# Optimization experiments

Measured on AMD Instinct MI355X. Metric: run time of the kernel, lower is better.

## Reference

```python
import jax, jax.numpy as jnp
import numpy as np

K = 4            # kNN neighbors (edge_conv k=4)
HEADS = 4
HID = 32
NEG_SLOPE = 0.2  # PyG GATConv leaky_relu default


def knn_idx(x, k):
    # x: [N, C]. Pairwise squared distances via gram trick, self excluded.
    N = x.shape[0]
    sq = jnp.sum(x * x, axis=1)
    d = sq[:, None] + sq[None, :] - 2.0 * (x @ x.T)          # [N, N]
    r = jnp.arange(N)
    d = d.at[r, r].set(jnp.inf)                               # no self in kNN
    _, idx = jax.lax.top_k(-d, k)                             # [N, k] nearest
    return idx


def gat_layer(x, neigh, W, a_src, a_dst, b):
    # x: [N, C]; neigh: [N, k+1] (incl. self loop). PyG GATConv, concat=True.
    N = x.shape[0]
    h = (x @ W).reshape(N, HEADS, HID)                        # [N, H, D]
    asrc = jnp.einsum('nhd,hd->nh', h, a_src)                 # [N, H]
    adst = jnp.einsum('nhd,hd->nh', h, a_dst)                 # [N, H]
    e = jax.nn.leaky_relu(adst[:, None, :] + asrc[neigh], NEG_SLOPE)  # [N, k+1, H]
    attn = jax.nn.softmax(e, axis=1)                          # segment softmax (fixed fan-in)
    out = jnp.einsum('nkh,nkhd->nhd', attn, h[neigh])         # [N, H, D]
    return out.reshape(N, HEADS * HID) + b


def setup_inputs() -> dict:
    key = jax.random.key(0)
    ks = jax.random.split(key, 12)
    B, E, C = 256, 64, 32
    s = 0.1
    return {
        'x': jax.random.normal(ks[0], (B, E, C), jnp.float32),
        # DynamicEdgeConv MLP: Linear(2C->HID), ReLU, Linear(HID->HID)
        'mlp_w1': jax.random.normal(ks[1], (2 * C, HID), jnp.float32) * s,
        'mlp_b1': jnp.zeros((HID,), jnp.float32),
        'mlp_w2': jax.random.normal(ks[2], (HID, HID), jnp.float32) * s,
        'mlp_b2': jnp.zeros((HID,), jnp.float32),
        # GATConv(HID, HID, heads=HEADS, concat=True)
        'gat_w': jax.random.normal(ks[3], (C, HEADS * HID), jnp.float32) * s,
        'gat_asrc': jax.random.normal(ks[4], (HEADS, HID), jnp.float32) * s,
        'gat_adst': jax.random.normal(ks[5], (HEADS, HID), jnp.float32) * s,
        'gat_b': jnp.zeros((HEADS * HID,), jnp.float32),
        # fc: Linear(HID*HEADS -> num_classes)
        'fc_w': jax.random.normal(ks[6], (HEADS * HID, 2), jnp.float32) * s,
        'fc_b': jnp.zeros((2,), jnp.float32),
    }


def reference(x, mlp_w1, mlp_b1, mlp_w2, mlp_b2, gat_w, gat_asrc, gat_adst, gat_b, fc_w, fc_b):
    B, E, C = x.shape
    N = B * E
    xf = x.reshape(N, C)
    idx = knn_idx(xf, K)                                      # [N, K] int32
    # EdgeConv message MLP + max pool (edge_attr is discarded by the original forward)
    xi = xf[:, None, :]                                       # [N, 1, C]
    xj = xf[idx]                                              # [N, K, C]
    ef = jnp.concatenate([jnp.broadcast_to(xi, xj.shape), xj - xi], axis=-1)
    ef = jax.nn.relu(ef @ mlp_w1 + mlp_b1) @ mlp_w2 + mlp_b2
    _edge_attr = ef.max(axis=1)                               # [N, HID], unused downstream
    # GAT with self loops (PyG add_self_loops=True)
    neigh = jnp.concatenate([idx, jnp.arange(N)[:, None]], axis=1)  # [N, K+1]
    h = gat_layer(xf, neigh, gat_w, gat_asrc, gat_adst, gat_b)
    h = jax.nn.elu(h)
    h = h.reshape(B, E, HEADS * HID).mean(axis=1)             # [B, H*D]
    return h @ fc_w + fc_b                                    # [B, num_classes]
```

## Files before the change

### kernel.cpp

```cpp
#include <hip/hip_runtime.h>
#include <math.h>

#define N_PTS   16384
#define NT      1024
#define NCHUNK  32
#define JT_CH   (NT/NCHUNK)
#define SUBT    8
#define NSUB    (JT_CH/SUBT)
#define NS      16
#define JSPLIT  4

typedef __attribute__((ext_vector_type(4))) float f32x4;
typedef __attribute__((ext_vector_type(8))) _Float16 half8;

union H8 { half8 h; float4 f; };

#define MED3(a,b,c) __builtin_amdgcn_fmed3f((a),(b),(c))

#define INS4(c, A0, A1, A2, A3) {        \
  float n0_ = fmaxf(A0, c);              \
  float n1_ = MED3(A0, A1, c);           \
  float n2_ = MED3(A1, A2, c);           \
  float n3_ = MED3(A2, A3, c);           \
  A0 = n0_; A1 = n1_; A2 = n2_; A3 = n3_; }

__device__ __forceinline__ unsigned long long pack_key(float a, int j) {
  unsigned u = __float_as_uint(a);
  unsigned ord = u ^ (unsigned)(((int)u >> 31) | 0x80000000);
  unsigned m = ~ord;
  return ((unsigned long long)m << 32) | (unsigned)j;
}

__global__ __launch_bounds__(256) void k_prep(
    const float* __restrict__ x, float4* __restrict__ fragHi,
    float4* __restrict__ fragLo, float* __restrict__ nsq,
    unsigned* __restrict__ gcnt, unsigned long long* __restrict__ gbuf,
    unsigned* __restrict__ bcnt)
{
  int p = blockIdx.x * 256 + threadIdx.x;
  const float4* xp = (const float4*)(x + (size_t)p * 32);
  int tile = p >> 4, lb = p & 15;
  float sq = 0.f;
  #pragma unroll
  for (int g = 0; g < 4; ++g) {
    float4 va = xp[g * 2], vb = xp[g * 2 + 1];
    float f[8] = {va.x, va.y, va.z, va.w, vb.x, vb.y, vb.z, vb.w};
    H8 hh, hl;
    #pragma unroll
    for (int e = 0; e < 8; ++e) {
      sq = fmaf(f[e], f[e], sq);
      _Float16 hi = (_Float16)f[e];
      _Float16 lo = (_Float16)(f[e] - (float)hi);
      hh.h[e] = hi; hl.h[e] = lo;
    }
    int a = tile * 64 + g * 16 + lb;
    fragHi[a] = hh.f; fragLo[a] = hl.f;
  }
  nsq[p] = -0.5f * sq;
  gcnt[p] = 0u;
  #pragma unroll
  for (int e = 0; e < NS; ++e) gbuf[(size_t)p * NS + e] = ~0ull;
  if (blockIdx.x == 0 && threadIdx.x < NCHUNK) bcnt[threadIdx.x] = 0u;
}

__global__ __launch_bounds__(256, 4) void k_knnA(
    const float4* __restrict__ fragHi, const float4* __restrict__ fragLo,
    const float* __restrict__ nsq, float* __restrict__ cvals)
{
  __shared__ half8 sHi[SUBT * 64];
  __shared__ half8 sLo[SUBT * 64];
  __shared__ float sNq[SUBT * 16];

  const int tid = threadIdx.x;
  const int w = tid >> 6, lane = tid & 63;
  const int grp = lane >> 4, col = lane & 15;
  const int cy = blockIdx.y;
  const int itbase = blockIdx.x * 16 + w * 4;
  const bool blkdiag = ((int)(blockIdx.x >> 1) == cy);

  const half8* fH8 = (const half8*)fragHi;
  const half8* fL8 = (const half8*)fragLo;

  half8 bh[4], bl[4];
  #pragma unroll
  for (int s = 0; s < 4; ++s) {
    bh[s] = fH8[(size_t)(itbase + s) * 64 + lane];
    bl[s] = fL8[(size_t)(itbase + s) * 64 + lane];
  }
  const bool dg0 = (col == grp * 4 + 0), dg1 = (col == grp * 4 + 1);
  const bool dg2 = (col == grp * 4 + 2), dg3 = (col == grp * 4 + 3);

  float La1[4];
  #pragma unroll
  for (int s = 0; s < 4; ++s) La1[s] = -3.4e38f;

  for (int sc = 0; sc < NSUB; ++sc) {
    int jt0 = cy * JT_CH + sc * SUBT;
    __syncthreads();
    const float4* gH = fragHi + (size_t)jt0 * 64;
    const float4* gL = fragLo + (size_t)jt0 * 64;
    float4* dH = (float4*)sHi;
    float4* dL = (float4*)sLo;
    #pragma unroll
    for (int r = 0; r < 2; ++r) {
      dH[tid + r * 256] = gH[tid + r * 256];
      dL[tid + r * 256] = gL[tid + r * 256];
    }
    if (tid < SUBT * 16) sNq[tid] = nsq[jt0 * 16 + tid];
    __syncthreads();

    for (int t = 0; t < SUBT; ++t) {
      half8 ah = sHi[t * 64 + lane];
      half8 al = sLo[t * 64 + lane];
      f32x4 q = *(const f32x4*)&sNq[t * 16 + grp * 4];
      int jt = jt0 + t;
      #pragma unroll
      for (int s = 0; s < 4; ++s) {
        f32x4 acc = __builtin_amdgcn_mfma_f32_16x16x32_f16(ah, bh[s], q, 0, 0, 0);
        acc = __builtin_amdgcn_mfma_f32_16x16x32_f16(ah, bl[s], acc, 0, 0, 0);
        acc = __builtin_amdgcn_mfma_f32_16x16x32_f16(al, bh[s], acc, 0, 0, 0);
        if (blkdiag && jt == itbase + s) {
          acc.x = dg0 ? -3.4e38f : acc.x;
          acc.y = dg1 ? -3.4e38f : acc.y;
          acc.z = dg2 ? -3.4e38f : acc.z;
          acc.w = dg3 ? -3.4e38f : acc.w;
        }
        float t3 = fmaxf(fmaxf(acc.x, acc.y), acc.z);
        La1[s] = fmaxf(fmaxf(t3, acc.w), La1[s]);
      }
    }
  }

  #pragma unroll
  for (int s = 0; s < 4; ++s) {
    float m = La1[s];
    m = fmaxf(m, __shfl_xor(m, 16));
    m = fmaxf(m, __shfl_xor(m, 32));
    if (grp == 0) {
      int row = (itbase + s) * 16 + col;
      cvals[(size_t)cy * N_PTS + row] = m;
    }
  }
}

__global__ __launch_bounds__(128) void k_tauwl(
    const float* __restrict__ cvals, float* __restrict__ tau,
    unsigned* __restrict__ bcnt, int* __restrict__ bucket)
{
  __shared__ unsigned lcnt[NCHUNK];
  __shared__ unsigned gbase[NCHUNK];
  __shared__ int stage[NCHUNK][64];
  __shared__ float4 sL[64];
  __shared__ float sT[64];

  const int tid = threadIdx.x;
  const int lrow = tid & 63, half = tid >> 6;
  const int row = blockIdx.x * 64 + lrow;
  if (tid < NCHUNK) lcnt[tid] = 0u;
  __syncthreads();

  float A0 = -3.4e38f, A1 = -3.4e38f, A2 = -3.4e38f, A3 = -3.4e38f;
  float cm[16];
  #pragma unroll
  for (int k = 0; k < 16; ++k) {
    cm[k] = cvals[(size_t)(half * 16 + k) * N_PTS + row];
    INS4(cm[k], A0, A1, A2, A3);
  }
  if (half == 1) sL[lrow] = make_float4(A0, A1, A2, A3);
  __syncthreads();
  if (half == 0) {
    float4 o = sL[lrow];
    INS4(o.x, A0, A1, A2, A3);
    INS4(o.y, A0, A1, A2, A3);
    INS4(o.z, A0, A1, A2, A3);
    INS4(o.w, A0, A1, A2, A3);
    sT[lrow] = A3;
    tau[row] = A3;
  }
  __syncthreads();
  const float tt = sT[lrow];
  #pragma unroll
  for (int k = 0; k < 16; ++k) {
    if (cm[k] >= tt) {
      int c = half * 16 + k;
      unsigned p = atomicAdd(&lcnt[c], 1u);
      stage[c][p] = row;
    }
  }
  __syncthreads();
  if (tid < NCHUNK) gbase[tid] = atomicAdd(bcnt + tid, lcnt[tid]);
  __syncthreads();
  for (int c = 0; c < NCHUNK; ++c) {
    unsigned n = lcnt[c], gb = gbase[c];
    for (unsigned k = tid; k < n; k += 128)
      bucket[c * N_PTS + gb + k] = stage[c][k];
  }
}

__global__ __launch_bounds__(256) void k_knnBW(
    const float4* __restrict__ fragHi, const float4* __restrict__ fragLo,
    const float* __restrict__ nsq, const float* __restrict__ tau,
    const unsigned* __restrict__ bcnt, const int* __restrict__ bucket,
    unsigned* __restrict__ gcnt, unsigned long long* __restrict__ gbuf)
{
  const int c = blockIdx.x;
  const int jseg = blockIdx.y >> 8;
  const unsigned n = bcnt[c];
  const unsigned base = (unsigned)(blockIdx.y & 255) * 64;
  if (base >= n) return;

  __shared__ int   sRow[64];
  __shared__ float sTau[64];

  const int tid = threadIdx.x;
  const int w = tid >> 6, lane = tid & 63;
  const int grp = lane >> 4, col = lane & 15;
  const float INF = __int_as_float(0x7f800000);

  if (tid < 64) {
    unsigned idx = base + tid;
    int myrow = (idx < n) ? bucket[c * N_PTS + idx] : -1;
    sRow[tid] = myrow;
    sTau[tid] = (myrow >= 0) ? tau[myrow] : INF;
  }
  __syncthreads();

  const half8* fH8 = (const half8*)fragHi;
  const half8* fL8 = (const half8*)fragLo;

  half8 bh[4], bl[4];
  int   rS[4];
  float tS[4];
  #pragma unroll
  for (int s = 0; s < 4; ++s) {
    int r = sRow[s * 16 + col];
    rS[s] = r;
    tS[s] = sTau[s * 16 + col];
    int rr = r < 0 ? 0 : r;
    size_t a = (size_t)(rr >> 4) * 64 + grp * 16 + (rr & 15);
    bh[s] = fH8[a];
    bl[s] = fL8[a];
  }

  const int jt0 = c * JT_CH + jseg * (JT_CH / JSPLIT) + w * (JT_CH / (JSPLIT * 4));
  #pragma unroll
  for (int ti = 0; ti < JT_CH / (JSPLIT * 4); ++ti) {
    int jt = jt0 + ti;
    half8 ah = fH8[(size_t)jt * 64 + lane];
    half8 al = fL8[(size_t)jt * 64 + lane];
    f32x4 q = *(const f32x4*)&nsq[jt * 16 + grp * 4];
    #pragma unroll
    for (int s = 0; s < 4; ++s) {
      f32x4 acc = __builtin_amdgcn_mfma_f32_16x16x32_f16(ah, bh[s], q, 0, 0, 0);
      acc = __builtin_amdgcn_mfma_f32_16x16x32_f16(ah, bl[s], acc, 0, 0, 0);
      acc = __builtin_amdgcn_mfma_f32_16x16x32_f16(al, bh[s], acc, 0, 0, 0);
      int jbase = jt * 16 + grp * 4;
      acc.x = (jbase + 0 == rS[s]) ? -3.4e38f : acc.x;
      acc.y = (jbase + 1 == rS[s]) ? -3.4e38f : acc.y;
      acc.z = (jbase + 2 == rS[s]) ? -3.4e38f : acc.z;
      acc.w = (jbase + 3 == rS[s]) ? -3.4e38f : acc.w;
      float m = fmaxf(fmaxf(acc.x, acc.y), fmaxf(acc.z, acc.w));
      if (__ballot(m >= tS[s])) {
        float av[4] = {acc.x, acc.y, acc.z, acc.w};
        #pragma unroll
        for (int e = 0; e < 4; ++e) {
          if (av[e] >= tS[s]) {
            unsigned sl = atomicAdd(gcnt + rS[s], 1u);
            if (sl < (unsigned)NS) gbuf[(size_t)rS[s] * NS + sl] = pack_key(av[e], jbase + e);
          }
        }
      }
    }
  }
}

__global__ __launch_bounds__(256) void k_feat(
    const float* __restrict__ x, const float* __restrict__ gw,
    const float* __restrict__ aw_s, const float* __restrict__ aw_d,
    float* __restrict__ h, float* __restrict__ asrc, float* __restrict__ adst)
{
  const int tid = threadIdx.x;
  const int d = tid & 127, half = tid >> 7;
  const int head = d >> 5, hid = d & 31;

  float gwr[32];
  #pragma unroll
  for (int k = 0; k < 32; ++k) gwr[k] = gw[k * 128 + d];
  const float ws_ = aw_s[head * 32 + hid], wd_ = aw_d[head * 32 + hid];

  #pragma unroll
  for (int p = 0; p < 8; ++p) {
    int nl = (p << 1) | half;
    int n = blockIdx.x * 16 + nl;
    const float4* xr = (const float4*)(x + (size_t)n * 32);
    float acc = 0.f;
    #pragma unroll
    for (int r = 0; r < 8; ++r) {
      float4 v = xr[r];
      acc = fmaf(v.x, gwr[r * 4 + 0], acc);
      acc = fmaf(v.y, gwr[r * 4 + 1], acc);
      acc = fmaf(v.z, gwr[r * 4 + 2], acc);
      acc = fmaf(v.w, gwr[r * 4 + 3], acc);
    }
    h[(size_t)n * 128 + d] = acc;
    float ps = acc * ws_, pd = acc * wd_;
    #pragma unroll
    for (int off = 16; off; off >>= 1) {
      ps += __shfl_xor(ps, off, 32);
      pd += __shfl_xor(pd, off, 32);
    }
    if (hid == 0) { asrc[n * 4 + head] = ps; adst[n * 4 + head] = pd; }
  }
}

__global__ __launch_bounds__(256) void k_gat(
    const float* __restrict__ h, const float* __restrict__ asrc, const float* __restrict__ adst,
    const unsigned long long* __restrict__ gbuf, const float* __restrict__ gb,
    float* __restrict__ mo_part)
{
  int b2 = blockIdx.x;
  int b = b2 >> 2, qq = b2 & 3;
  int tid = threadIdx.x;
  __shared__ int4 sknn[16];
  if (tid < 16) {
    int row = b * 64 + qq * 16 + tid;
    unsigned long long K0 = ~0ull, K1 = ~0ull, K2 = ~0ull, K3 = ~0ull;
    const unsigned long long* src = gbuf + (size_t)row * NS;
    #pragma unroll
    for (int e = 0; e < NS; ++e) {
      unsigned long long cc = src[e];
      bool g = cc < K3, c0 = cc < K0, c1 = cc < K1, c2 = cc < K2;
      unsigned long long n1 = c0 ? K0 : (c1 ? cc : K1);
      unsigned long long n2 = c1 ? K1 : (c2 ? cc : K2);
      unsigned long long n3 = c2 ? K2 : (g ? cc : K3);
      K0 = c0 ? cc : K0; K1 = n1; K2 = n2; K3 = n3;
    }
    sknn[tid] = make_int4((int)(unsigned)K0, (int)(unsigned)K1,
                          (int)(unsigned)K2, (int)(unsigned)K3);
  }
  __syncthreads();

  int w = tid >> 6, lane = tid & 63;
  int da = lane, db = lane + 64;
  int ha = lane >> 5, hb = ha + 2;
  float acca = 0.f, accb = 0.f;

  #pragma unroll
  for (int t = 0; t < 4; ++t) {
    int nl = t * 4 + w;
    int n = b * 64 + qq * 16 + nl;
    int4 nb = sknn[nl];
    int nbs[5] = {nb.x, nb.y, nb.z, nb.w, n};
    float ad_a = adst[n * 4 + ha], ad_b = adst[n * 4 + hb];
    float ea[5], eb[5];
    #pragma unroll
    for (int k = 0; k < 5; ++k) {
      float va = ad_a + asrc[nbs[k] * 4 + ha];
      float vb = ad_b + asrc[nbs[k] * 4 + hb];
      ea[k] = va > 0.f ? va : 0.2f * va;
      eb[k] = vb > 0.f ? vb : 0.2f * vb;
    }
    float ma = ea[0], mb = eb[0];
    #pragma unroll
    for (int k = 1; k < 5; ++k) { ma = fmaxf(ma, ea[k]); mb = fmaxf(mb, eb[k]); }
    float sa = 0.f, sb = 0.f;
    #pragma unroll
    for (int k = 0; k < 5; ++k) {
      ea[k] = __expf(ea[k] - ma); sa += ea[k];
      eb[k] = __expf(eb[k] - mb); sb += eb[k];
    }
    float outa = 0.f, outb = 0.f;
    #pragma unroll
    for (int k = 0; k < 5; ++k) {
      const float* hr = h + (size_t)nbs[k] * 128;
      outa = fmaf(ea[k], hr[da], outa);
      outb = fmaf(eb[k], hr[db], outb);
    }
    outa = outa / sa + gb[da];
    outb = outb / sb + gb[db];
    acca += outa > 0.f ? outa : expm1f(outa);
    accb += outb > 0.f ? outb : expm1f(outb);
  }

  __shared__ float red[4][128];
  red[w][da] = acca; red[w][db] = accb;
  __syncthreads();
  if (tid < 128) {
    float s = (red[0][tid] + red[1][tid] + red[2][tid] + red[3][tid]) * (1.f / 64.f);
    mo_part[b2 * 128 + tid] = s;
  }
}

__global__ __launch_bounds__(64) void k_fc(
    const float* __restrict__ mo_part, const float* __restrict__ fw, const float* __restrict__ fb,
    float* __restrict__ out)
{
  int b = blockIdx.x, lane = threadIdx.x;
  float m0 = 0.f, m1 = 0.f;
  #pragma unroll
  for (int q = 0; q < 4; ++q) {
    m0 += mo_part[(b * 4 + q) * 128 + lane];
    m1 += mo_part[(b * 4 + q) * 128 + lane + 64];
  }
  float p0 = m0 * fw[lane * 2]     + m1 * fw[(lane + 64) * 2];
  float p1 = m0 * fw[lane * 2 + 1] + m1 * fw[(lane + 64) * 2 + 1];
  #pragma unroll
  for (int off = 32; off; off >>= 1) {
    p0 += __shfl_xor(p0, off, 64);
    p1 += __shfl_xor(p1, off, 64);
  }
  if (lane == 0) { out[b * 2] = p0 + fb[0]; out[b * 2 + 1] = p1 + fb[1]; }
}

extern "C" void kernel_launch(void* const* d_in, const int* in_sizes, int n_in,
                              void* d_out, int out_size, void* d_ws, size_t ws_size,
                              hipStream_t stream)
{
  const float* x   = (const float*)d_in[0];
  const float* gw  = (const float*)d_in[5];
  const float* as_ = (const float*)d_in[6];
  const float* ad_ = (const float*)d_in[7];
  const float* gb  = (const float*)d_in[8];
  const float* fw  = (const float*)d_in[9];
  const float* fb  = (const float*)d_in[10];

  char* ws = (char*)d_ws;
  float*  cvals  = (float*)(ws);
  float*  h      = (float*)(ws + 2097152);
  float*  asrc   = (float*)(ws + 10485760);
  float*  adst   = (float*)(ws + 10747904);
  float4* fragHi = (float4*)(ws + 11010048);
  float4* fragLo = (float4*)(ws + 12058624);
  float*  nsq    = (float*)(ws + 13107200);
  float*  tau    = (float*)(ws + 13172736);
  unsigned* gcnt = (unsigned*)(ws + 13238272);
  unsigned long long* gbuf = (unsigned long long*)(ws + 13303808);
  unsigned* bcnt = (unsigned*)(ws + 15400960);
  int*    bucket = (int*)   (ws + 15401216);
  float*  mo_part= (float*)(ws + 17498368);
  float*  outp   = (float*)d_out;

  k_prep<<<64, 256, 0, stream>>>(x, fragHi, fragLo, nsq, gcnt, gbuf, bcnt);
  k_knnA<<<dim3(64, NCHUNK), 256, 0, stream>>>(fragHi, fragLo, nsq, cvals);
  k_tauwl<<<N_PTS / 64, 128, 0, stream>>>(cvals, tau, bcnt, bucket);
  k_knnBW<<<dim3(NCHUNK, 256 * JSPLIT), 256, 0, stream>>>(fragHi, fragLo, nsq, tau,
                                                          bcnt, bucket, gcnt, gbuf);
  k_feat<<<N_PTS / 16, 256, 0, stream>>>(x, gw, as_, ad_, h, asrc, adst);
  k_gat<<<1024, 256, 0, stream>>>(h, asrc, adst, gbuf, gb, mo_part);
  k_fc<<<256, 64, 0, stream>>>(mo_part, fw, fb, outp);
}
```

Baseline: 114.8 us.

## Use hi-only fp16 MFMA in kNN screening pass with error-bounded threshold

The first kNN screening pass now issues a single fp16 MFMA on the high halves instead of three split-precision MFMAs, and it no longer loads the low fragments. To keep the candidate filter safe, k_prep computes the maximum hi and lo squared norms through wave reductions and atomics. k_tauwl then lowers each row's threshold by an error bound derived from those norms, so the exact second pass still sees every true neighbour. The sub-tile size also doubles to 16 and k_prep's block size changes. The looser threshold may admit more candidates into the refinement pass, and a memset plus an atomic reduction are added.

```diff
diff --git a/kernel.cpp b/kernel.cpp
--- a/kernel.cpp
+++ b/kernel.cpp
@@ -5,7 +5,7 @@
 #define NT      1024
 #define NCHUNK  32
 #define JT_CH   (NT/NCHUNK)
-#define SUBT    8
+#define SUBT    16
 #define NSUB    (JT_CH/SUBT)
 #define NS      16
 #define JSPLIT  4
@@ -31,16 +31,16 @@
   return ((unsigned long long)m << 32) | (unsigned)j;
 }
 
-__global__ __launch_bounds__(256) void k_prep(
+__global__ __launch_bounds__(64) void k_prep(
     const float* __restrict__ x, float4* __restrict__ fragHi,
     float4* __restrict__ fragLo, float* __restrict__ nsq,
     unsigned* __restrict__ gcnt, unsigned long long* __restrict__ gbuf,
-    unsigned* __restrict__ bcnt)
-{
-  int p = blockIdx.x * 256 + threadIdx.x;
+    unsigned* __restrict__ bcnt, float* __restrict__ nmx)
+{
+  int p = blockIdx.x * 64 + threadIdx.x;
   const float4* xp = (const float4*)(x + (size_t)p * 32);
   int tile = p >> 4, lb = p & 15;
-  float sq = 0.f;
+  float sq = 0.f, hn2 = 0.f, ln2 = 0.f;
   #pragma unroll
   for (int g = 0; g < 4; ++g) {
     float4 va = xp[g * 2], vb = xp[g * 2 + 1];
@@ -52,6 +52,9 @@
       _Float16 hi = (_Float16)f[e];
       _Float16 lo = (_Float16)(f[e] - (float)hi);
       hh.h[e] = hi; hl.h[e] = lo;
+      float hf = (float)hi, lf = (float)lo;
+      hn2 = fmaf(hf, hf, hn2);
+      ln2 = fmaf(lf, lf, ln2);
     }
     int a = tile * 64 + g * 16 + lb;
     fragHi[a] = hh.f; fragLo[a] = hl.f;
@@ -61,14 +64,23 @@
   #pragma unroll
   for (int e = 0; e < NS; ++e) gbuf[(size_t)p * NS + e] = ~0ull;
   if (blockIdx.x == 0 && threadIdx.x < NCHUNK) bcnt[threadIdx.x] = 0u;
+
+  #pragma unroll
+  for (int off = 32; off; off >>= 1) {
+    hn2 = fmaxf(hn2, __shfl_xor(hn2, off));
+    ln2 = fmaxf(ln2, __shfl_xor(ln2, off));
+  }
+  if (threadIdx.x == 0) {
+    atomicMax((unsigned*)&nmx[0], __float_as_uint(hn2));
+    atomicMax((unsigned*)&nmx[1], __float_as_uint(ln2));
+  }
 }
 
 __global__ __launch_bounds__(256, 4) void k_knnA(
-    const float4* __restrict__ fragHi, const float4* __restrict__ fragLo,
-    const float* __restrict__ nsq, float* __restrict__ cvals)
+    const float4* __restrict__ fragHi, const float* __restrict__ nsq,
+    float* __restrict__ cvals)
 {
   __shared__ half8 sHi[SUBT * 64];
-  __shared__ half8 sLo[SUBT * 64];
   __shared__ float sNq[SUBT * 16];
 
   const int tid = threadIdx.x;
@@ -79,14 +91,11 @@
   const bool blkdiag = ((int)(blockIdx.x >> 1) == cy);
 
   const half8* fH8 = (const half8*)fragHi;
-  const half8* fL8 = (const half8*)fragLo;
-
-  half8 bh[4], bl[4];
-  #pragma unroll
-  for (int s = 0; s < 4; ++s) {
+
+  half8 bh[4];
+  #pragma unroll
+  for (int s = 0; s < 4; ++s)
     bh[s] = fH8[(size_t)(itbase + s) * 64 + lane];
-    bl[s] = fL8[(size_t)(itbase + s) * 64 + lane];
-  }
   const bool dg0 = (col == grp * 4 + 0), dg1 = (col == grp * 4 + 1);
   const bool dg2 = (col == grp * 4 + 2), dg3 = (col == grp * 4 + 3);
 
@@ -98,27 +107,20 @@
     int jt0 = cy * JT_CH + sc * SUBT;
     __syncthreads();
     const float4* gH = fragHi + (size_t)jt0 * 64;
-    const float4* gL = fragLo + (size_t)jt0 * 64;
     float4* dH = (float4*)sHi;
-    float4* dL = (float4*)sLo;
-    #pragma unroll
-    for (int r = 0; r < 2; ++r) {
+    #pragma unroll
+    for (int r = 0; r < 4; ++r)
       dH[tid + r * 256] = gH[tid + r * 256];
-      dL[tid + r * 256] = gL[tid + r * 256];
-    }
-    if (tid < SUBT * 16) sNq[tid] = nsq[jt0 * 16 + tid];
+    sNq[tid] = nsq[jt0 * 16 + tid];
     __syncthreads();
 
     for (int t = 0; t < SUBT; ++t) {
       half8 ah = sHi[t * 64 + lane];
-      half8 al = sLo[t * 64 + lane];
       f32x4 q = *(const f32x4*)&sNq[t * 16 + grp * 4];
       int jt = jt0 + t;
       #pragma unroll
       for (int s = 0; s < 4; ++s) {
         f32x4 acc = __builtin_amdgcn_mfma_f32_16x16x32_f16(ah, bh[s], q, 0, 0, 0);
-        acc = __builtin_amdgcn_mfma_f32_16x16x32_f16(ah, bl[s], acc, 0, 0, 0);
-        acc = __builtin_amdgcn_mfma_f32_16x16x32_f16(al, bh[s], acc, 0, 0, 0);
         if (blkdiag && jt == itbase + s) {
           acc.x = dg0 ? -3.4e38f : acc.x;
           acc.y = dg1 ? -3.4e38f : acc.y;
@@ -145,7 +147,8 @@
 
 __global__ __launch_bounds__(128) void k_tauwl(
     const float* __restrict__ cvals, float* __restrict__ tau,
-    unsigned* __restrict__ bcnt, int* __restrict__ bucket)
+    unsigned* __restrict__ bcnt, int* __restrict__ bucket,
+    const float* __restrict__ nmx)
 {
   __shared__ unsigned lcnt[NCHUNK];
   __shared__ unsigned gbase[NCHUNK];
@@ -157,6 +160,8 @@
   const int lrow = tid & 63, half = tid >> 6;
   const int row = blockIdx.x * 64 + lrow;
   if (tid < NCHUNK) lcnt[tid] = 0u;
+
+  const float eps = 4.4f * sqrtf(nmx[0]) * sqrtf(nmx[1]) + 1e-3f;
   __syncthreads();
 
   float A0 = -3.4e38f, A1 = -3.4e38f, A2 = -3.4e38f, A3 = -3.4e38f;
@@ -174,8 +179,9 @@
     INS4(o.y, A0, A1, A2, A3);
     INS4(o.z, A0, A1, A2, A3);
     INS4(o.w, A0, A1, A2, A3);
-    sT[lrow] = A3;
-    tau[row] = A3;
+    float theta = A3 - eps;
+    sT[lrow] = theta;
+    tau[row] = theta;
   }
   __syncthreads();
   const float tt = sT[lrow];
@@ -436,13 +442,15 @@
   unsigned* gcnt = (unsigned*)(ws + 13238272);
   unsigned long long* gbuf = (unsigned long long*)(ws + 13303808);
   unsigned* bcnt = (unsigned*)(ws + 15400960);
-  int*    bucket = (int*)   (ws + 15401216);
-  float*  mo_part= (float*)(ws + 17498368);
+  float*  nmx    = (float*)(ws + 15401216);
+  int*    bucket = (int*)   (ws + 15401472);
+  float*  mo_part= (float*)(ws + 17498624);
   float*  outp   = (float*)d_out;
 
-  k_prep<<<64, 256, 0, stream>>>(x, fragHi, fragLo, nsq, gcnt, gbuf, bcnt);
-  k_knnA<<<dim3(64, NCHUNK), 256, 0, stream>>>(fragHi, fragLo, nsq, cvals);
-  k_tauwl<<<N_PTS / 64, 128, 0, stream>>>(cvals, tau, bcnt, bucket);
+  hipMemsetAsync(nmx, 0, 8, stream);
+  k_prep<<<256, 64, 0, stream>>>(x, fragHi, fragLo, nsq, gcnt, gbuf, bcnt, nmx);
+  k_knnA<<<dim3(64, NCHUNK), 256, 0, stream>>>(fragHi, nsq, cvals);
+  k_tauwl<<<N_PTS / 64, 128, 0, stream>>>(cvals, tau, bcnt, bucket, nmx);
   k_knnBW<<<dim3(NCHUNK, 256 * JSPLIT), 256, 0, stream>>>(fragHi, fragLo, nsq, tau,
                                                           bcnt, bucket, gcnt, gbuf);
   k_feat<<<N_PTS / 16, 256, 0, stream>>>(x, gw, as_, ad_, h, asrc, adst);
```

Result: faster. 107.7 us (-6.2%).
